# Kernel tuning notes

Measured on AMD Instinct MI355X. Metric: run time of the kernel, lower is better.

The kernel has to match this reference:

```python
import jax, jax.numpy as jnp
import numpy as np

CH = 128
GROUPS = 8
EPS = 1e-5


def setup_inputs() -> dict:
    key = jax.random.key(0)
    ks = jax.random.split(key, 12)
    b, c, h, w = 16, CH, 64, 64
    x = jax.random.normal(ks[0], (b, c, h, w), dtype=jnp.float32)
    s = 1.0 / np.sqrt(c)
    return {
        "x": x,
        "gn_w": jnp.ones((c,), jnp.float32),
        "gn_b": jnp.zeros((c,), jnp.float32),
        "wq": jax.random.normal(ks[1], (c, c), jnp.float32) * s,
        "bq": jax.random.normal(ks[2], (c,), jnp.float32) * 0.01,
        "wk": jax.random.normal(ks[3], (c, c), jnp.float32) * s,
        "bk": jax.random.normal(ks[4], (c,), jnp.float32) * 0.01,
        "wv": jax.random.normal(ks[5], (c, c), jnp.float32) * s,
        "bv": jax.random.normal(ks[6], (c,), jnp.float32) * 0.01,
        "wf": jax.random.normal(ks[7], (c, c), jnp.float32) * s,
        "bf": jax.random.normal(ks[8], (c,), jnp.float32) * 0.01,
    }


def _group_norm(x, gamma, beta):
    b, c, h, w = x.shape
    xg = x.reshape(b, GROUPS, -1)  # [b, g, (c/g)*h*w]
    mean = xg.mean(axis=-1, keepdims=True)
    var = xg.var(axis=-1, keepdims=True)
    xn = ((xg - mean) * jax.lax.rsqrt(var + EPS)).reshape(b, c, h, w)
    return xn * gamma[None, :, None, None] + beta[None, :, None, None]


def reference(x, gn_w, gn_b, wq, bq, wk, bk, wv, bv, wf, bf):
    b, c, h, w = x.shape
    x_gn = _group_norm(x, gn_w, gn_b)
    xf = x_gn.reshape(b, c, h * w)  # [b, c, n]
    # 1x1 convs == per-position channel matmuls
    q = jnp.einsum('oc,bcn->bon', wq, xf) + bq[None, :, None]
    k = jnp.einsum('oc,bcn->bon', wk, xf) + bk[None, :, None]
    v = jnp.einsum('oc,bcn->bon', wv, xf) + bv[None, :, None]
    scale = c ** (-0.5)
    attn = jnp.einsum('bci,bcj->bij', q, k) * scale  # [b, n, n]
    attn = jax.nn.softmax(attn, axis=-1)
    # out[b,c,i] = sum_j v[b,c,j] * attn[b,i,j]
    o = jnp.einsum('bcj,bij->bci', v, attn)
    of = jnp.einsum('oc,bcn->bon', wf, o) + bf[None, :, None]
    return of.reshape(b, c, h, w) + x
```

## Files before the change

kernel.cpp:

```cpp
#include <hip/hip_runtime.h>

#define NB   16
#define NC   128
#define NPOS 4096

typedef short bf16x8 __attribute__((ext_vector_type(8)));
typedef float f32x4  __attribute__((ext_vector_type(4)));
typedef float f32x16 __attribute__((ext_vector_type(16)));
typedef unsigned int u32x4 __attribute__((ext_vector_type(4)));
typedef unsigned int u32x2 __attribute__((ext_vector_type(2)));

#define SCF 0.12751743075095855f

static __device__ __forceinline__ unsigned short f2bf(float f) {
    unsigned int u = __builtin_bit_cast(unsigned int, f);
    u += 0x7FFFu + ((u >> 16) & 1u);
    return (unsigned short)(u >> 16);
}

static __device__ __forceinline__ unsigned int pkbf(float hi, float lo) {
    return __builtin_amdgcn_perm(__builtin_bit_cast(unsigned int, hi),
                                 __builtin_bit_cast(unsigned int, lo), 0x07060302u);
}

static __device__ __forceinline__ void mk_bfrag_pair(const float* pp, bf16x8* dst) {
    #pragma unroll
    for (int c2 = 0; c2 < 2; ++c2) {
        int rb = c2 * 8;
        unsigned int A0 = pkbf(pp[rb + 1], pp[rb + 0]);
        unsigned int A1 = pkbf(pp[rb + 3], pp[rb + 2]);
        unsigned int B0 = pkbf(pp[rb + 5], pp[rb + 4]);
        unsigned int B1 = pkbf(pp[rb + 7], pp[rb + 6]);
        u32x2 r0 = __builtin_amdgcn_permlane32_swap(A0, B0, false, false);
        u32x2 r1 = __builtin_amdgcn_permlane32_swap(A1, B1, false, false);
        u32x4 f;
        f[0] = r0[0]; f[1] = r1[0]; f[2] = r0[1]; f[3] = r1[1];
        dst[c2] = __builtin_bit_cast(bf16x8, f);
    }
}

static __device__ __forceinline__ void stage_tile(unsigned short* lds, const unsigned short* g,
                                                  int t, int w) {
    #pragma unroll
    for (int c = 0; c < 4; ++c) {
        __builtin_amdgcn_global_load_lds(
            (const __attribute__((address_space(1))) unsigned int*)(g + c * 2048 + t * 8),
            (__attribute__((address_space(3))) unsigned int*)(lds + c * 2048 + w * 512),
            16, 0, 0);
    }
}

__global__ void wconv_kernel(const float* __restrict__ wq, const float* __restrict__ wk,
                             const float* __restrict__ wv, const float* __restrict__ wf,
                             unsigned short* __restrict__ oq, unsigned short* __restrict__ ok,
                             unsigned short* __restrict__ ov, unsigned short* __restrict__ of) {
    int i = blockIdx.x * 256 + threadIdx.x;
    oq[i] = f2bf(wq[i]); ok[i] = f2bf(wk[i]); ov[i] = f2bf(wv[i]); of[i] = f2bf(wf[i]);
}

__global__ void gnstat_kernel(const float* __restrict__ x, float* __restrict__ mean,
                              float* __restrict__ rstd) {
    int bg = blockIdx.x;
    const float* p = x + (size_t)bg * 65536;
    int t = threadIdx.x;
    float s = 0.f, q = 0.f;
    for (int it = 0; it < 64; ++it) {
        f32x4 v = *(const f32x4*)(p + it * 1024 + t * 4);
        s += v[0] + v[1] + v[2] + v[3];
        q += v[0] * v[0] + v[1] * v[1] + v[2] * v[2] + v[3] * v[3];
    }
    for (int m = 1; m < 64; m <<= 1) { s += __shfl_xor(s, m); q += __shfl_xor(q, m); }
    __shared__ float ls[4], lq[4];
    int w = t >> 6;
    if ((t & 63) == 0) { ls[w] = s; lq[w] = q; }
    __syncthreads();
    if (t == 0) {
        s = ls[0] + ls[1] + ls[2] + ls[3];
        q = lq[0] + lq[1] + lq[2] + lq[3];
        float mu  = s * (1.0f / 65536.0f);
        float var = q * (1.0f / 65536.0f) - mu * mu;
        mean[bg] = mu;
        rstd[bg] = rsqrtf(var + 1e-5f);
    }
}

__global__ __launch_bounds__(256) void qkv_kernel(
    const float* __restrict__ x, const float* __restrict__ gnw, const float* __restrict__ gnb,
    const float* __restrict__ mean, const float* __restrict__ rstd,
    const unsigned short* __restrict__ wqb, const unsigned short* __restrict__ wkb,
    const unsigned short* __restrict__ wvb,
    const float* __restrict__ bq, const float* __restrict__ bk, const float* __restrict__ bv,
    unsigned short* __restrict__ qT, unsigned short* __restrict__ Kf, unsigned short* __restrict__ Vf) {
    __shared__ __attribute__((aligned(16))) unsigned short xn[64 * 136];
    __shared__ __attribute__((aligned(16))) unsigned short bnc[64 * 128];
    const int b = blockIdx.y, i0 = blockIdx.x * 64, jt = blockIdx.x;
    const int t = threadIdx.x;
    {
        int iL = (t & 15) * 4;
        int cb = (t >> 4) * 2;
        for (int cg = 0; cg < 4; ++cg) {
            int c = cg * 32 + cb;
            int g = c >> 4;
            float mu = mean[b * 8 + g], rs = rstd[b * 8 + g];
            float ga0 = gnw[c] * rs,     be0 = gnb[c]     - mu * ga0;
            float ga1 = gnw[c + 1] * rs, be1 = gnb[c + 1] - mu * ga1;
            const float* p0 = x + ((size_t)(b * NC + c)) * NPOS + i0 + iL;
            f32x4 v0 = *(const f32x4*)p0;
            f32x4 v1 = *(const f32x4*)(p0 + NPOS);
            for (int e = 0; e < 4; ++e) {
                unsigned int u = (unsigned)f2bf(v0[e] * ga0 + be0) |
                                 ((unsigned)f2bf(v1[e] * ga1 + be1) << 16);
                *(unsigned int*)&xn[(iL + e) * 136 + c] = u;
            }
        }
    }
    __syncthreads();

    const int lane = t & 63, w = t >> 6, quad = lane >> 4, li = lane & 15;

    bf16x8 ax[4];
    for (int kc = 0; kc < 4; ++kc)
        ax[kc] = *(const bf16x8*)&xn[(w * 16 + li) * 136 + kc * 32 + quad * 8];

    for (int wt = 0; wt < 2; ++wt) {
        const unsigned short* W = wt ? wkb : wqb;
        const float* bias = wt ? bk : bq;
        const float osc = wt ? 1.0f : SCF;
        for (int nt = 0; nt < 8; ++nt) {
            f32x4 d = {0.f, 0.f, 0.f, 0.f};
            for (int kc = 0; kc < 4; ++kc) {
                bf16x8 bw = *(const bf16x8*)&W[(nt * 16 + li) * 128 + kc * 32 + quad * 8];
                d = __builtin_amdgcn_mfma_f32_16x16x32_bf16(ax[kc], bw, d, 0, 0, 0);
            }
            float bb = bias[nt * 16 + li];
            int o = nt * 16 + li;
            for (int rr = 0; rr < 4; ++rr) {
                int i = w * 16 + quad * 4 + rr;
                bnc[i * 128 + (((o >> 3) ^ (i & 7)) << 3) + (o & 7)] = f2bf((d[rr] + bb) * osc);
            }
        }
        __syncthreads();
        if (wt == 0) {
            unsigned short* dst = qT + ((size_t)b * NPOS + i0) * NC + t * 32;
            int i = t >> 2;
            for (int s = 0; s < 4; ++s) {
                int cc = (t & 3) * 4 + s;
                *(bf16x8*)(dst + s * 8) = *(const bf16x8*)&bnc[i * 128 + ((cc ^ (i & 7)) << 3)];
            }
        } else {
            unsigned short* dst = Kf + ((size_t)(b * 64 + jt)) * 8192 + t * 32;
            int F = t >> 4, jtile = F >> 3, kc = F & 7;
            for (int s = 0; s < 4; ++s) {
                int L = (t * 4 + s) & 63;
                int i = jtile * 32 + (L & 31);
                int cc = kc * 2 + (L >> 5);
                *(bf16x8*)(dst + s * 8) = *(const bf16x8*)&bnc[i * 128 + ((cc ^ (i & 7)) << 3)];
            }
        }
        __syncthreads();
    }

    bf16x8 av[2][4];
    for (int mt = 0; mt < 2; ++mt)
        for (int kc = 0; kc < 4; ++kc)
            av[mt][kc] = *(const bf16x8*)&wvb[((w * 2 + mt) * 16 + li) * 128 + kc * 32 + quad * 8];
    for (int nt = 0; nt < 4; ++nt) {
        bf16x8 bx[4];
        for (int kc = 0; kc < 4; ++kc)
            bx[kc] = *(const bf16x8*)&xn[(nt * 16 + li) * 136 + kc * 32 + quad * 8];
        for (int mt = 0; mt < 2; ++mt) {
            f32x4 d = {0.f, 0.f, 0.f, 0.f};
            for (int kc = 0; kc < 4; ++kc)
                d = __builtin_amdgcn_mfma_f32_16x16x32_bf16(av[mt][kc], bx[kc], d, 0, 0, 0);
            int o0 = (w * 2 + mt) * 16 + quad * 4;
            int j = nt * 16 + li;
            for (int rr = 0; rr < 4; ++rr) {
                int c = o0 + rr;
                bnc[c * 64 + (((j >> 3) ^ (c & 7)) << 3) + (j & 7)] = f2bf(d[rr] + bv[c]);
            }
        }
    }
    __syncthreads();
    {
        unsigned short* dst = Vf + ((size_t)(b * 64 + jt)) * 8192 + t * 32;
        int F = t >> 4, ct = F >> 2, kc2 = F & 3;
        for (int s = 0; s < 4; ++s) {
            int L = (t * 4 + s) & 63;
            int c = ct * 32 + (L & 31);
            int jc = kc2 * 2 + (L >> 5);
            *(bf16x8*)(dst + s * 8) = *(const bf16x8*)&bnc[c * 64 + ((jc ^ (c & 7)) << 3)];
        }
    }
}

__global__ __launch_bounds__(256, 2) void flash_kernel(
    const unsigned short* __restrict__ qT, const unsigned short* __restrict__ Kf,
    const unsigned short* __restrict__ Vf, const unsigned short* __restrict__ wfb,
    const float* __restrict__ bf_, const float* __restrict__ x, float* __restrict__ out) {
    __shared__ __attribute__((aligned(16))) unsigned short Kv[2][8192];
    __shared__ __attribute__((aligned(16))) unsigned short Vv[2][8192];
    const int idx = blockIdx.x;
    const int b = (idx & 7) * 2 + ((idx >> 3) & 1);
    const int rg = idx >> 4;
    const int t = threadIdx.x, lane = t & 63, w = t >> 6;
    const int il = lane & 31, h = lane >> 5;
    const int iw = (rg * 4 + w) * 32;

    const unsigned short* Kb = Kf + ((size_t)b * 64) * 8192;
    const unsigned short* Vb = Vf + ((size_t)b * 64) * 8192;

    stage_tile(&Kv[0][0], Kb, t, w);
    stage_tile(&Kv[1][0], Kb + 8192, t, w);
    stage_tile(&Vv[0][0], Vb, t, w);

    bf16x8 qb[8];
    #pragma unroll
    for (int kc = 0; kc < 8; ++kc)
        qb[kc] = *(const bf16x8*)&qT[((size_t)b * NPOS + iw + il) * NC + kc * 16 + h * 8];

    bf16x8 ones;
    {
        u32x4 o; o[0] = o[1] = o[2] = o[3] = 0x3F803F80u;
        ones = __builtin_bit_cast(bf16x8, o);
    }

    f32x16 acc[4], accl;
    #pragma unroll
    for (int ct = 0; ct < 4; ++ct)
        #pragma unroll
        for (int q = 0; q < 16; ++q) acc[ct][q] = 0.f;
    #pragma unroll
    for (int q = 0; q < 16; ++q) accl[q] = 0.f;

    __syncthreads();

    f32x16 st[2];
    #pragma unroll
    for (int u = 0; u < 2; ++u)
        #pragma unroll
        for (int q = 0; q < 16; ++q) st[u][q] = 0.f;
    {
        const unsigned short* kl = &Kv[0][0] + lane * 8;
        __builtin_amdgcn_s_setprio(1);
        #pragma unroll
        for (int kc = 0; kc < 8; ++kc) {
            bf16x8 k0 = *(const bf16x8*)(kl + kc * 512);
            bf16x8 k1 = *(const bf16x8*)(kl + (8 + kc) * 512);
            st[0] = __builtin_amdgcn_mfma_f32_32x32x16_bf16(k0, qb[kc], st[0], 0, 0, 0);
            st[1] = __builtin_amdgcn_mfma_f32_32x32x16_bf16(k1, qb[kc], st[1], 0, 0, 0);
        }
        __builtin_amdgcn_s_setprio(0);
    }
    __syncthreads();

    for (int jt = 0; jt < 64; ++jt) {
        if (jt < 62) stage_tile(&Kv[jt & 1][0], Kb + (size_t)(jt + 2) * 8192, t, w);
        if (jt < 63) stage_tile(&Vv[(jt + 1) & 1][0], Vb + (size_t)(jt + 1) * 8192, t, w);

        #pragma unroll
        for (int q = 0; q < 16; ++q) {
            st[0][q] = __builtin_amdgcn_exp2f(st[0][q]);
            st[1][q] = __builtin_amdgcn_exp2f(st[1][q]);
        }

        bf16x8 pfrag[4];
        mk_bfrag_pair((const float*)&st[0], &pfrag[0]);
        mk_bfrag_pair((const float*)&st[1], &pfrag[2]);

        const unsigned short* vl = &Vv[jt & 1][0] + lane * 8;
        const unsigned short* kl = &Kv[(jt + 1) & 1][0] + lane * 8;

        #pragma unroll
        for (int u = 0; u < 2; ++u)
            #pragma unroll
            for (int q = 0; q < 16; ++q) st[u][q] = 0.f;

        __builtin_amdgcn_s_setprio(1);
        #pragma unroll
        for (int i = 0; i < 16; ++i) {
            const int ct = i & 3, kc2 = i >> 2;
            bf16x8 vfm = *(const bf16x8*)(vl + (ct * 4 + kc2) * 512);
            acc[ct] = __builtin_amdgcn_mfma_f32_32x32x16_bf16(vfm, pfrag[kc2], acc[ct], 0, 0, 0);
            const int ch = i & 1, kc = i >> 1;
            bf16x8 kx = *(const bf16x8*)(kl + (ch * 8 + kc) * 512);
            st[ch] = __builtin_amdgcn_mfma_f32_32x32x16_bf16(kx, qb[kc], st[ch], 0, 0, 0);
            if ((i & 3) == 3)
                accl = __builtin_amdgcn_mfma_f32_32x32x16_bf16(ones, pfrag[i >> 2], accl, 0, 0, 0);
        }
        __builtin_amdgcn_s_setprio(0);

        __syncthreads();
    }

    const float lr = accl[0];
    bf16x8 obf[8];
    {
        float inv = __builtin_amdgcn_rcpf(lr) * 1.001953125f;
        #pragma unroll
        for (int ct = 0; ct < 4; ++ct) {
            float pp[16];
            #pragma unroll
            for (int q = 0; q < 16; ++q) pp[q] = acc[ct][q] * inv;
            mk_bfrag_pair(pp, &obf[ct * 2]);
        }
    }

    #pragma unroll
    for (int ot = 0; ot < 4; ++ot) {
        bf16x8 wfA[8];
        #pragma unroll
        for (int kc = 0; kc < 8; ++kc)
            wfA[kc] = *(const bf16x8*)&wfb[(ot * 32 + il) * 128 + kc * 16 + h * 8];
        f32x16 d;
        #pragma unroll
        for (int q = 0; q < 16; ++q) d[q] = 0.f;
        #pragma unroll
        for (int kc = 0; kc < 8; ++kc)
            d = __builtin_amdgcn_mfma_f32_32x32x16_bf16(wfA[kc], obf[kc], d, 0, 0, 0);
        const int gi = iw + il;
        #pragma unroll
        for (int q = 0; q < 16; ++q) {
            int o = ot * 32 + (q & 3) + 8 * (q >> 2) + 4 * h;
            size_t a = ((size_t)(b * NC + o)) * NPOS + gi;
            out[a] = d[q] + bf_[o] + x[a];
        }
    }
}

extern "C" void kernel_launch(void* const* d_in, const int* in_sizes, int n_in,
                              void* d_out, int out_size, void* d_ws, size_t ws_size,
                              hipStream_t stream) {
    const float* x   = (const float*)d_in[0];
    const float* gnw = (const float*)d_in[1];
    const float* gnb = (const float*)d_in[2];
    const float* wq  = (const float*)d_in[3];
    const float* bq  = (const float*)d_in[4];
    const float* wk  = (const float*)d_in[5];
    const float* bk  = (const float*)d_in[6];
    const float* wv  = (const float*)d_in[7];
    const float* bv  = (const float*)d_in[8];
    const float* wf  = (const float*)d_in[9];
    const float* bf_ = (const float*)d_in[10];
    float* out = (float*)d_out;

    char* ws = (char*)d_ws;
    float* mean = (float*)(ws + 0);
    float* rstd = (float*)(ws + 512);
    unsigned short* wqb = (unsigned short*)(ws + 1024);
    unsigned short* wkb = wqb + 16384;
    unsigned short* wvb = wkb + 16384;
    unsigned short* wfb = wvb + 16384;
    unsigned short* qT  = (unsigned short*)(ws + 132096);
    unsigned short* Kf  = qT + (size_t)NB * NPOS * NC;
    unsigned short* Vf  = Kf + (size_t)NB * NPOS * NC;

    wconv_kernel<<<64, 256, 0, stream>>>(wq, wk, wv, wf, wqb, wkb, wvb, wfb);
    gnstat_kernel<<<128, 256, 0, stream>>>(x, mean, rstd);
    dim3 g(64, 16);
    qkv_kernel<<<g, 256, 0, stream>>>(x, gnw, gnb, mean, rstd, wqb, wkb, wvb, bq, bk, bv, qT, Kf, Vf);
    flash_kernel<<<512, 256, 0, stream>>>(qT, Kf, Vf, wfb, bf_, x, out);
}
```

Measured before the change: 295.9 us.

## Process two query tiles per wave to reuse K/V fragments in flash kernel

Each wave now handles 64 query rows (two 32-row groups) instead of 32, so every K and V LDS fragment load feeds two MFMAs. The grid is halved to 256 blocks and launch bounds drop to one block per SIMD group to leave room for the doubled accumulators. The loop is also restructured into a two-stage software pipeline with ping-pong score buffers, so the next tile's QK^T is computed before the current tile's exp and PV. The cost is much higher register pressure, lower occupancy, and fewer blocks than there are CUs on a 256-CU part, which may leave compute units idle.

```diff
diff --git a/kernel.cpp b/kernel.cpp
--- a/kernel.cpp
+++ b/kernel.cpp
@@ -193,7 +193,59 @@
     }
 }
 
-__global__ __launch_bounds__(256, 2) void flash_kernel(
+static __device__ __forceinline__ void flash_iter(
+    int jt, f32x16 (&stC)[4], f32x16 (&stN)[4], const f32x16& z16,
+    const bf16x8 (&qb)[2][8], const bf16x8& ones,
+    f32x16 (&acc)[2][4], f32x16 (&accl)[2],
+    unsigned short (*Kv)[8192], unsigned short (*Vv)[8192],
+    const unsigned short* Kb, const unsigned short* Vb, int t, int w, int lane) {
+    if (jt < 62) stage_tile(&Kv[jt & 1][0], Kb + (size_t)(jt + 2) * 8192, t, w);
+    if (jt < 63) stage_tile(&Vv[(jt + 1) & 1][0], Vb + (size_t)(jt + 1) * 8192, t, w);
+
+    const unsigned short* kl = &Kv[(jt + 1) & 1][0] + lane * 8;
+    const unsigned short* vl = &Vv[jt & 1][0] + lane * 8;
+
+    __builtin_amdgcn_s_setprio(1);
+    #pragma unroll
+    for (int kc = 0; kc < 8; ++kc) {
+        bf16x8 k0 = *(const bf16x8*)(kl + kc * 512);
+        bf16x8 k1 = *(const bf16x8*)(kl + (8 + kc) * 512);
+        stN[0] = __builtin_amdgcn_mfma_f32_32x32x16_bf16(k0, qb[0][kc], kc ? stN[0] : z16, 0, 0, 0);
+        stN[1] = __builtin_amdgcn_mfma_f32_32x32x16_bf16(k1, qb[0][kc], kc ? stN[1] : z16, 0, 0, 0);
+        stN[2] = __builtin_amdgcn_mfma_f32_32x32x16_bf16(k0, qb[1][kc], kc ? stN[2] : z16, 0, 0, 0);
+        stN[3] = __builtin_amdgcn_mfma_f32_32x32x16_bf16(k1, qb[1][kc], kc ? stN[3] : z16, 0, 0, 0);
+    }
+    __builtin_amdgcn_s_setprio(0);
+
+    #pragma unroll
+    for (int u = 0; u < 4; ++u)
+        #pragma unroll
+        for (int q = 0; q < 16; ++q) stC[u][q] = __builtin_amdgcn_exp2f(stC[u][q]);
+
+    bf16x8 pfrag[2][4];
+    mk_bfrag_pair((const float*)&stC[0], &pfrag[0][0]);
+    mk_bfrag_pair((const float*)&stC[1], &pfrag[0][2]);
+    mk_bfrag_pair((const float*)&stC[2], &pfrag[1][0]);
+    mk_bfrag_pair((const float*)&stC[3], &pfrag[1][2]);
+
+    __builtin_amdgcn_s_setprio(1);
+    #pragma unroll
+    for (int i = 0; i < 16; ++i) {
+        const int ct = i & 3, kc2 = i >> 2;
+        bf16x8 vfm = *(const bf16x8*)(vl + (ct * 4 + kc2) * 512);
+        acc[0][ct] = __builtin_amdgcn_mfma_f32_32x32x16_bf16(vfm, pfrag[0][kc2], acc[0][ct], 0, 0, 0);
+        acc[1][ct] = __builtin_amdgcn_mfma_f32_32x32x16_bf16(vfm, pfrag[1][kc2], acc[1][ct], 0, 0, 0);
+        if ((i & 3) == 3) {
+            accl[0] = __builtin_amdgcn_mfma_f32_32x32x16_bf16(ones, pfrag[0][i >> 2], accl[0], 0, 0, 0);
+            accl[1] = __builtin_amdgcn_mfma_f32_32x32x16_bf16(ones, pfrag[1][i >> 2], accl[1], 0, 0, 0);
+        }
+    }
+    __builtin_amdgcn_s_setprio(0);
+
+    __syncthreads();
+}
+
+__global__ __launch_bounds__(256, 1) void flash_kernel(
     const unsigned short* __restrict__ qT, const unsigned short* __restrict__ Kf,
     const unsigned short* __restrict__ Vf, const unsigned short* __restrict__ wfb,
     const float* __restrict__ bf_, const float* __restrict__ x, float* __restrict__ out) {
@@ -204,7 +256,7 @@
     const int rg = idx >> 4;
     const int t = threadIdx.x, lane = t & 63, w = t >> 6;
     const int il = lane & 31, h = lane >> 5;
-    const int iw = (rg * 4 + w) * 32;
+    const int iw = (rg * 4 + w) * 64;
 
     const unsigned short* Kb = Kf + ((size_t)b * 64) * 8192;
     const unsigned short* Vb = Vf + ((size_t)b * 64) * 8192;
@@ -213,32 +265,36 @@
     stage_tile(&Kv[1][0], Kb + 8192, t, w);
     stage_tile(&Vv[0][0], Vb, t, w);
 
-    bf16x8 qb[8];
-    #pragma unroll
-    for (int kc = 0; kc < 8; ++kc)
-        qb[kc] = *(const bf16x8*)&qT[((size_t)b * NPOS + iw + il) * NC + kc * 16 + h * 8];
+    bf16x8 qb[2][8];
+    #pragma unroll
+    for (int ig = 0; ig < 2; ++ig)
+        #pragma unroll
+        for (int kc = 0; kc < 8; ++kc)
+            qb[ig][kc] = *(const bf16x8*)&qT[((size_t)b * NPOS + iw + ig * 32 + il) * NC + kc * 16 + h * 8];
 
     bf16x8 ones;
     {
         u32x4 o; o[0] = o[1] = o[2] = o[3] = 0x3F803F80u;
         ones = __builtin_bit_cast(bf16x8, o);
     }
-
-    f32x16 acc[4], accl;
-    #pragma unroll
-    for (int ct = 0; ct < 4; ++ct)
-        #pragma unroll
-        for (int q = 0; q < 16; ++q) acc[ct][q] = 0.f;
-    #pragma unroll
-    for (int q = 0; q < 16; ++q) accl[q] = 0.f;
-
-    __syncthreads();
-
-    f32x16 st[2];
-    #pragma unroll
-    for (int u = 0; u < 2; ++u)
-        #pragma unroll
-        for (int q = 0; q < 16; ++q) st[u][q] = 0.f;
+    f32x16 z16;
+    #pragma unroll
+    for (int q = 0; q < 16; ++q) z16[q] = 0.f;
+
+    f32x16 acc[2][4], accl[2];
+    #pragma unroll
+    for (int ig = 0; ig < 2; ++ig) {
+        #pragma unroll
+        for (int ct = 0; ct < 4; ++ct)
+            #pragma unroll
+            for (int q = 0; q < 16; ++q) acc[ig][ct][q] = 0.f;
+        #pragma unroll
+        for (int q = 0; q < 16; ++q) accl[ig][q] = 0.f;
+    }
+
+    __syncthreads();
+
+    f32x16 stA[4], stB[4];
     {
         const unsigned short* kl = &Kv[0][0] + lane * 8;
         __builtin_amdgcn_s_setprio(1);
@@ -246,62 +302,30 @@
         for (int kc = 0; kc < 8; ++kc) {
             bf16x8 k0 = *(const bf16x8*)(kl + kc * 512);
             bf16x8 k1 = *(const bf16x8*)(kl + (8 + kc) * 512);
-            st[0] = __builtin_amdgcn_mfma_f32_32x32x16_bf16(k0, qb[kc], st[0], 0, 0, 0);
-            st[1] = __builtin_amdgcn_mfma_f32_32x32x16_bf16(k1, qb[kc], st[1], 0, 0, 0);
+            stA[0] = __builtin_amdgcn_mfma_f32_32x32x16_bf16(k0, qb[0][kc], kc ? stA[0] : z16, 0, 0, 0);
+            stA[1] = __builtin_amdgcn_mfma_f32_32x32x16_bf16(k1, qb[0][kc], kc ? stA[1] : z16, 0, 0, 0);
+            stA[2] = __builtin_amdgcn_mfma_f32_32x32x16_bf16(k0, qb[1][kc], kc ? stA[2] : z16, 0, 0, 0);
+            stA[3] = __builtin_amdgcn_mfma_f32_32x32x16_bf16(k1, qb[1][kc], kc ? stA[3] : z16, 0, 0, 0);
         }
         __builtin_amdgcn_s_setprio(0);
     }
     __syncthreads();
 
-    for (int jt = 0; jt < 64; ++jt) {
-        if (jt < 62) stage_tile(&Kv[jt & 1][0], Kb + (size_t)(jt + 2) * 8192, t, w);
-        if (jt < 63) stage_tile(&Vv[(jt + 1) & 1][0], Vb + (size_t)(jt + 1) * 8192, t, w);
-
-        #pragma unroll
-        for (int q = 0; q < 16; ++q) {
-            st[0][q] = __builtin_amdgcn_exp2f(st[0][q]);
-            st[1][q] = __builtin_amdgcn_exp2f(st[1][q]);
-        }
-
-        bf16x8 pfrag[4];
-        mk_bfrag_pair((const float*)&st[0], &pfrag[0]);
-        mk_bfrag_pair((const float*)&st[1], &pfrag[2]);
-
-        const unsigned short* vl = &Vv[jt & 1][0] + lane * 8;
-        const unsigned short* kl = &Kv[(jt + 1) & 1][0] + lane * 8;
-
-        #pragma unroll
-        for (int u = 0; u < 2; ++u)
-            #pragma unroll
-            for (int q = 0; q < 16; ++q) st[u][q] = 0.f;
-
-        __builtin_amdgcn_s_setprio(1);
-        #pragma unroll
-        for (int i = 0; i < 16; ++i) {
-            const int ct = i & 3, kc2 = i >> 2;
-            bf16x8 vfm = *(const bf16x8*)(vl + (ct * 4 + kc2) * 512);
-            acc[ct] = __builtin_amdgcn_mfma_f32_32x32x16_bf16(vfm, pfrag[kc2], acc[ct], 0, 0, 0);
-            const int ch = i & 1, kc = i >> 1;
-            bf16x8 kx = *(const bf16x8*)(kl + (ch * 8 + kc) * 512);
-            st[ch] = __builtin_amdgcn_mfma_f32_32x32x16_bf16(kx, qb[kc], st[ch], 0, 0, 0);
-            if ((i & 3) == 3)
-                accl = __builtin_amdgcn_mfma_f32_32x32x16_bf16(ones, pfrag[i >> 2], accl, 0, 0, 0);
-        }
-        __builtin_amdgcn_s_setprio(0);
-
-        __syncthreads();
-    }
-
-    const float lr = accl[0];
-    bf16x8 obf[8];
-    {
-        float inv = __builtin_amdgcn_rcpf(lr) * 1.001953125f;
+    for (int jo = 0; jo < 32; ++jo) {
+        flash_iter(2 * jo,     stA, stB, z16, qb, ones, acc, accl, Kv, Vv, Kb, Vb, t, w, lane);
+        flash_iter(2 * jo + 1, stB, stA, z16, qb, ones, acc, accl, Kv, Vv, Kb, Vb, t, w, lane);
+    }
+
+    bf16x8 obf[2][8];
+    #pragma unroll
+    for (int ig = 0; ig < 2; ++ig) {
+        float inv = __builtin_amdgcn_rcpf(accl[ig][0]) * 1.001953125f;
         #pragma unroll
         for (int ct = 0; ct < 4; ++ct) {
             float pp[16];
             #pragma unroll
-            for (int q = 0; q < 16; ++q) pp[q] = acc[ct][q] * inv;
-            mk_bfrag_pair(pp, &obf[ct * 2]);
+            for (int q = 0; q < 16; ++q) pp[q] = acc[ig][ct][q] * inv;
+            mk_bfrag_pair(pp, &obf[ig][ct * 2]);
         }
     }
 
@@ -311,18 +335,21 @@
         #pragma unroll
         for (int kc = 0; kc < 8; ++kc)
             wfA[kc] = *(const bf16x8*)&wfb[(ot * 32 + il) * 128 + kc * 16 + h * 8];
-        f32x16 d;
-        #pragma unroll
-        for (int q = 0; q < 16; ++q) d[q] = 0.f;
-        #pragma unroll
-        for (int kc = 0; kc < 8; ++kc)
-            d = __builtin_amdgcn_mfma_f32_32x32x16_bf16(wfA[kc], obf[kc], d, 0, 0, 0);
-        const int gi = iw + il;
-        #pragma unroll
-        for (int q = 0; q < 16; ++q) {
-            int o = ot * 32 + (q & 3) + 8 * (q >> 2) + 4 * h;
-            size_t a = ((size_t)(b * NC + o)) * NPOS + gi;
-            out[a] = d[q] + bf_[o] + x[a];
+        #pragma unroll
+        for (int ig = 0; ig < 2; ++ig) {
+            f32x16 d;
+            #pragma unroll
+            for (int q = 0; q < 16; ++q) d[q] = 0.f;
+            #pragma unroll
+            for (int kc = 0; kc < 8; ++kc)
+                d = __builtin_amdgcn_mfma_f32_32x32x16_bf16(wfA[kc], obf[ig][kc], d, 0, 0, 0);
+            const int gi = iw + ig * 32 + il;
+            #pragma unroll
+            for (int q = 0; q < 16; ++q) {
+                int o = ot * 32 + (q & 3) + 8 * (q >> 2) + 4 * h;
+                size_t a = ((size_t)(b * NC + o)) * NPOS + gi;
+                out[a] = d[q] + bf_[o] + x[a];
+            }
         }
     }
 }
@@ -358,5 +385,5 @@
     gnstat_kernel<<<128, 256, 0, stream>>>(x, mean, rstd);
     dim3 g(64, 16);
     qkv_kernel<<<g, 256, 0, stream>>>(x, gnw, gnb, mean, rstd, wqb, wkb, wvb, bq, bk, bv, qT, Kf, Vf);
-    flash_kernel<<<512, 256, 0, stream>>>(qT, Kf, Vf, wfb, bf_, x, out);
-}
+    flash_kernel<<<256, 256, 0, stream>>>(qT, Kf, Vf, wfb, bf_, x, out);
+}
```

Measured after the change: 298.1 us. Within noise of the previous version (+0.7%).
